# Performance work log

Measured on AMD Instinct MI355X. Metric: run time of the kernel, lower is better.

Reference implementation:

```python
import jax, jax.numpy as jnp
import numpy as np

MODES = (16, 16)
EMBED_DIM = 64
NUM_HEADS = 8


def spectral_conv(x, w):
    """FNO-style spectral conv. x: [B,S,Ci,H,W]; w: [Ci,Co,mx,my,2] (real/imag)."""
    wc = w[..., 0] + 1j * w[..., 1]
    H, W = x.shape[-2], x.shape[-1]
    mx, my = wc.shape[2], wc.shape[3]
    xf = jnp.fft.rfft2(x)                                   # [B,S,Ci,H,W//2+1]
    of = jnp.einsum('bsixy,ioxy->bsoxy', xf[..., :mx, :my], wc)
    out_f = jnp.zeros(x.shape[:2] + (wc.shape[1], H, W // 2 + 1), dtype=of.dtype)
    out_f = out_f.at[..., :mx, :my].set(of)
    return jnp.fft.irfft2(out_f, s=(H, W))


def log_cpb_bias(n_sub_x, n_sub_y, w1, b1, w2):
    """Swin-v2-style log-spaced continuous position bias -> [heads, S, S]."""
    cx = jnp.arange(n_sub_x, dtype=jnp.float32)
    cy = jnp.arange(n_sub_y, dtype=jnp.float32)
    coords = jnp.stack(jnp.meshgrid(cx, cy, indexing='ij'), axis=-1).reshape(-1, 2)
    rel = coords[:, None, :] - coords[None, :, :]           # [S,S,2]
    rel = jnp.sign(rel) * jnp.log1p(jnp.abs(rel))
    h = jax.nn.relu(rel @ w1 + b1)                          # [S,S,hidden]
    bias = h @ w2                                           # [S,S,heads]
    return jnp.transpose(bias, (2, 0, 1))


def _unflatten(f, num_heads, embed_dim):
    # [B,S,h*d,H,W] -> [B,h,S,d,H,W]
    B, S = f.shape[0], f.shape[1]
    f = f.reshape(B, S, num_heads, embed_dim, f.shape[-2], f.shape[-1])
    return jnp.transpose(f, (0, 2, 1, 3, 4, 5))


def setup_inputs() -> dict:
    key = jax.random.key(0)
    ks = jax.random.split(key, 9)
    B, S, D, H, W = 2, 64, EMBED_DIM, 32, 32
    hd = NUM_HEADS * D
    mx, my = MODES
    scale = 0.02
    return {
        'seq': jax.random.normal(ks[0], (B, S, D, H, W), dtype=jnp.float32),
        'wq': scale * jax.random.normal(ks[1], (D, hd, mx, my, 2), dtype=jnp.float32),
        'wk': scale * jax.random.normal(ks[2], (D, hd, mx, my, 2), dtype=jnp.float32),
        'wv': scale * jax.random.normal(ks[3], (D, hd, mx, my, 2), dtype=jnp.float32),
        'wo': scale * jax.random.normal(ks[4], (hd, D, mx, my, 2), dtype=jnp.float32),
        'cpb_w1': scale * jax.random.normal(ks[5], (2, D), dtype=jnp.float32),
        'cpb_b1': jnp.zeros((D,), dtype=jnp.float32),
        'cpb_w2': scale * jax.random.normal(ks[6], (D, NUM_HEADS), dtype=jnp.float32),
        'n_sub_x': 8,
        'n_sub_y': 8,
    }


def reference(seq, wq, wk, wv, wo, cpb_w1, cpb_b1, cpb_w2, n_sub_x, n_sub_y):
    q = _unflatten(spectral_conv(seq, wq), NUM_HEADS, EMBED_DIM)  # [B,h,S,d,H,W]
    k = _unflatten(spectral_conv(seq, wk), NUM_HEADS, EMBED_DIM)
    v = _unflatten(spectral_conv(seq, wv), NUM_HEADS, EMBED_DIM)

    bias = log_cpb_bias(n_sub_x, n_sub_y, cpb_w1, cpb_b1, cpb_w2)  # [h,S,S]

    d, H, W = q.shape[-3], q.shape[-2], q.shape[-1]
    scale = 1.0 / jnp.sqrt(jnp.asarray(d * H * W, dtype=q.dtype))
    scores = jnp.einsum('bhqdxy,bhkdxy->bhqk', q, k) * scale + bias[None]
    attn = jax.nn.softmax(scores, axis=-1)
    sa = jnp.einsum('bhqk,bhkdxy->bhqdxy', attn, v)          # [B,h,S,d,H,W]

    # _flatten: [B,h,S,d,H,W] -> [B,S,h*d,H,W]
    sa = jnp.transpose(sa, (0, 2, 1, 3, 4, 5))
    B, S = sa.shape[0], sa.shape[1]
    sa = sa.reshape(B, S, NUM_HEADS * EMBED_DIM, H, W)
    return spectral_conv(sa, wo)
```

## Files before the change

### kernel.cpp

```cpp
#include <hip/hip_runtime.h>

#define TWO_PI 6.28318530717958647692f

#define NH 8
#define CH 128
#define NCH 2

#define OFF_XM   0ull
#define OFF_WTA  (OFF_XM + 8388608ull)
#define OFF_WTB  (OFF_WTA + 16777216ull)
#define OFF_PO   (OFF_WTB + 16777216ull)
#define OFF_ATTN (OFF_PO + 16777216ull)
#define WS_TOTAL (OFF_ATTN + 262144ull)

typedef short bf16x8 __attribute__((ext_vector_type(8)));
typedef float f32x4 __attribute__((ext_vector_type(4)));
#define MFMA_B16(a, b, c) __builtin_amdgcn_mfma_f32_16x16x32_bf16(a, b, c, 0, 0, 0)

__device__ __forceinline__ float bl(unsigned u) { return __uint_as_float(u << 16); }
__device__ __forceinline__ unsigned short f2b(float f) {
    unsigned u = __float_as_uint(f);
    return (unsigned short)((u + 0x7fffu + ((u >> 16) & 1u)) >> 16);
}
__device__ __forceinline__ unsigned pack2(float lo, float hi) {
    return (unsigned)f2b(lo) | ((unsigned)f2b(hi) << 16);
}

__device__ __forceinline__ bf16x8 mkfrag(const unsigned* __restrict__ Wt, int co_l, int ri,
                                         int ci0, bool dc) {
    unsigned a0 = Wt[(ci0 + 0) * 64 + (co_l ^ (ci0 + 0))];
    unsigned a1 = Wt[(ci0 + 1) * 64 + (co_l ^ (ci0 + 1))];
    unsigned a2 = Wt[(ci0 + 2) * 64 + (co_l ^ (ci0 + 2))];
    unsigned a3 = Wt[(ci0 + 3) * 64 + (co_l ^ (ci0 + 3))];
    uint4 r;
    if (ri) {
        if (dc) { r.x = 0u; r.y = 0u; r.z = 0u; r.w = 0u; }
        else {
            r.x = (a0 >> 16) | (a0 << 16); r.y = (a1 >> 16) | (a1 << 16);
            r.z = (a2 >> 16) | (a2 << 16); r.w = (a3 >> 16) | (a3 << 16);
        }
    } else {
        r.x = a0 ^ 0x80000000u; r.y = a1 ^ 0x80000000u;
        r.z = a2 ^ 0x80000000u; r.w = a3 ^ 0x80000000u;
    }
    return __builtin_bit_cast(bf16x8, r);
}

__global__ __launch_bounds__(256) void k_transpose2(const float* __restrict__ srcA, unsigned* __restrict__ dstA, int kindA,
                                                    const float* __restrict__ srcB, unsigned* __restrict__ dstB, int kindB,
                                                    int m0) {
    const float* in = (blockIdx.z == 0) ? srcA : srcB;
    unsigned* outp = (blockIdx.z == 0) ? dstA : dstB;
    int kind = (blockIdx.z == 0) ? kindA : kindB;
    __shared__ unsigned T[16][65];
    int tid = threadIdx.x;
    int r0 = blockIdx.x * 64;
    int ci, h;
    if (kind == 2) { h = r0 >> 12; ci = (r0 >> 6) & 63; }
    else           { ci = r0 >> 9; h = (r0 >> 6) & 7; }
    int ml0 = blockIdx.y * 16;
    int u = (m0 + ml0) >> 4;
    const float2* in2 = (const float2*)in;
    #pragma unroll
    for (int p = 0; p < 4; ++p) {
        int f = tid + p * 256;
        int row = f >> 4, mc = f & 15;
        float fac = (kind == 0) ? (mc > 0 ? 1.41421356f : (u > 0 ? 0.70710678f : 1.f))
                  : (kind == 1) ? (mc > 0 ? 1.f : (u > 0 ? 0.5f : 1.f)) : 1.f;
        float2 v = in2[(size_t)(r0 + row) * 256 + m0 + ml0 + mc];
        T[mc][row] = pack2(v.x * fac, v.y * fac);
    }
    __syncthreads();
    #pragma unroll
    for (int p = 0; p < 4; ++p) {
        int f = tid + p * 256;
        int ml = f >> 6, co = f & 63;
        outp[((size_t)((ml0 + ml) * 8 + h) << 12) + ci * 64 + co] = T[ml][co];
    }
}

__global__ __launch_bounds__(256) void k_rfft_y(const float* __restrict__ seq,
                                                float2* __restrict__ T) {
    __shared__ float c32[32], s32[32];
    __shared__ float fld[32][33];
    int tid = threadIdx.x;
    int bc = blockIdx.x;
    if (tid < 32) { float s, c; __sincosf(TWO_PI * tid / 32.0f, &s, &c); c32[tid] = c; s32[tid] = s; }
    float4 v = ((const float4*)(seq + (size_t)bc * 1024))[tid];
    int x = tid >> 3, y4 = (tid & 7) * 4;
    fld[x][y4] = v.x; fld[x][y4 + 1] = v.y; fld[x][y4 + 2] = v.z; fld[x][y4 + 3] = v.w;
    __syncthreads();
    float2* op = T + (size_t)bc * 512;
    #pragma unroll
    for (int p = 0; p < 2; ++p) {
        int e = tid + p * 256;
        int xx = e >> 4, vv = e & 15;
        float sr = 0.f, si = 0.f;
        #pragma unroll
        for (int y = 0; y < 32; ++y) {
            float f = fld[xx][y];
            int ph = (vv * y) & 31;
            sr = fmaf(f, c32[ph], sr);
            si = fmaf(-f, s32[ph], si);
        }
        float2 t; t.x = sr; t.y = si;
        op[e] = t;
    }
}

__global__ __launch_bounds__(256) void k_rfft_x(const float2* __restrict__ T,
                                                unsigned short* __restrict__ XM) {
    __shared__ float c32[32], s32[32];
    __shared__ float2 t[8][512];
    int tid = threadIdx.x;
    int cig = blockIdx.x;
    int bs = blockIdx.y;
    if (tid < 32) { float s, c; __sincosf(TWO_PI * tid / 32.0f, &s, &c); c32[tid] = c; s32[tid] = s; }
    const float4* src = (const float4*)(T + ((size_t)bs * 64 + cig * 8) * 512);
    #pragma unroll
    for (int p = 0; p < 8; ++p) {
        int idx = tid + p * 256;
        float4 w = src[idx];
        int ch = idx >> 8, r2 = idx & 255;
        float2 t0; t0.x = w.x; t0.y = w.y;
        float2 t1; t1.x = w.z; t1.y = w.w;
        t[ch][r2 * 2] = t0; t[ch][r2 * 2 + 1] = t1;
    }
    __syncthreads();
    int u = tid >> 4, vv = tid & 15;
    unsigned outw[8];
    for (int ch = 0; ch < 8; ++ch) {
        float xr = 0.f, xi = 0.f;
        #pragma unroll
        for (int x = 0; x < 32; ++x) {
            float2 tv = t[ch][x * 16 + vv];
            int ph = (u * x) & 31;
            float c = c32[ph], s = s32[ph];
            xr += tv.x * c + tv.y * s;
            xi += tv.y * c - tv.x * s;
        }
        outw[ch] = pack2(xr, xi);
    }
    uint4* op = (uint4*)(XM + (((size_t)tid * 128 + bs) * 64 + cig * 8) * 2);
    uint4 a, b;
    a.x = outw[0]; a.y = outw[1]; a.z = outw[2]; a.w = outw[3];
    b.x = outw[4]; b.y = outw[5]; b.z = outw[6]; b.w = outw[7];
    op[0] = a; op[1] = b;
}

__global__ __launch_bounds__(512) void k_qks(const unsigned short* __restrict__ XM,
                                             const unsigned* __restrict__ WQ,
                                             const unsigned* __restrict__ WK,
                                             float* __restrict__ part, int mbase) {
    __shared__ __align__(16) unsigned char Xs[16384];
    __shared__ __align__(16) unsigned Wq[4096];
    __shared__ __align__(16) unsigned Wk[4096];
    __shared__ __align__(16) unsigned char Qs[16384];
    __shared__ __align__(16) unsigned char Ks[16384];
    int tid = threadIdx.x;
    int mg = blockIdx.x, h = blockIdx.y, b = blockIdx.z;
    int lane = tid & 63, w = tid >> 6;
    int lr = lane & 15, lg = lane >> 4;
    int wr = w & 1, wc = w >> 1;
    int sxa = (lr & 7) << 4;
    int ri = lr & 1;
    f32x4 zf = {0.f, 0.f, 0.f, 0.f};
    f32x4 sacc[2];
    sacc[0] = zf; sacc[1] = zf;
    for (int mm = 0; mm < 4; ++mm) {
        int ml = mg * 4 + mm;
        int mode = mbase + ml;
        bool dc = (mode == 0);
        __syncthreads();
        {
            const unsigned short* xg = XM + ((size_t)mode * 128 + b * 64) * 128;
            #pragma unroll
            for (int p = 0; p < 2; ++p) {
                int g = tid + p * 512; int row = g >> 4, c16 = g & 15;
                uint4 v = *(const uint4*)(xg + row * 128 + c16 * 8);
                *(uint4*)(Xs + row * 256 + ((c16 * 16) ^ ((row & 7) << 4))) = v;
            }
        }
        {
            const unsigned* tq = WQ + ((size_t)(ml * 8 + h) << 12);
            const unsigned* tk = WK + ((size_t)(ml * 8 + h) << 12);
            #pragma unroll
            for (int p = 0; p < 16; ++p) {
                int idx = tid + p * 512;
                int r = idx & 4095;
                int ci = r >> 6, co = r & 63;
                if (idx < 4096) Wq[ci * 64 + (co ^ ci)] = tq[r];
                else            Wk[ci * 64 + (co ^ ci)] = tk[r];
            }
        }
        __syncthreads();
        {
            f32x4 qa[2][2], ka[2][2];
            #pragma unroll
            for (int m = 0; m < 2; ++m)
                #pragma unroll
                for (int n = 0; n < 2; ++n) { qa[m][n] = zf; ka[m][n] = zf; }
            #pragma unroll
            for (int ks = 0; ks < 4; ++ks) {
                int kb = (ks * 64 + lg * 16) ^ sxa;
                int ci0 = ks * 16 + lg * 4;
                bf16x8 a0 = *(const bf16x8*)(Xs + (wr * 32 + lr) * 256 + kb);
                bf16x8 a1 = *(const bf16x8*)(Xs + (wr * 32 + 16 + lr) * 256 + kb);
                #pragma unroll
                for (int n = 0; n < 2; ++n) {
                    int co_l = wc * 16 + n * 8 + (lr >> 1);
                    bf16x8 bq = mkfrag(Wq, co_l, ri, ci0, dc);
                    bf16x8 bk = mkfrag(Wk, co_l, ri, ci0, dc);
                    qa[0][n] = MFMA_B16(a0, bq, qa[0][n]);
                    qa[1][n] = MFMA_B16(a1, bq, qa[1][n]);
                    ka[0][n] = MFMA_B16(a0, bk, ka[0][n]);
                    ka[1][n] = MFMA_B16(a1, bk, ka[1][n]);
                }
            }
            #pragma unroll
            for (int m = 0; m < 2; ++m)
                #pragma unroll
                for (int n = 0; n < 2; ++n) {
                    int colb = (wc * 32 + n * 16 + lr) * 2;
                    #pragma unroll
                    for (int r = 0; r < 4; ++r) {
                        int row = wr * 32 + m * 16 + lg * 4 + r;
                        int swz = (row & 7) << 4;
                        *(unsigned short*)(Qs + row * 256 + (colb ^ swz)) = f2b(qa[m][n][r]);
                        *(unsigned short*)(Ks + row * 256 + (colb ^ swz)) = f2b(ka[m][n][r]);
                    }
                }
        }
        __syncthreads();
        {
            #pragma unroll
            for (int ks = 0; ks < 4; ++ks) {
                int kb = (ks * 64 + lg * 16) ^ sxa;
                bf16x8 a0 = *(const bf16x8*)(Qs + (wr * 32 + lr) * 256 + kb);
                bf16x8 a1 = *(const bf16x8*)(Qs + (wr * 32 + 16 + lr) * 256 + kb);
                bf16x8 b0 = *(const bf16x8*)(Ks + (wc * 16 + lr) * 256 + kb);
                sacc[0] = MFMA_B16(a0, b0, sacc[0]);
                sacc[1] = MFMA_B16(a1, b0, sacc[1]);
            }
        }
    }
    float* pp = part + (((size_t)((mbase >> 2) + mg) * 16 + b * 8 + h) << 12);
    #pragma unroll
    for (int m = 0; m < 2; ++m)
        #pragma unroll
        for (int r = 0; r < 4; ++r)
            pp[(wr * 32 + m * 16 + lg * 4 + r) * 64 + wc * 16 + lr] = sacc[m][r];
}

__global__ void k_softmax(const float* __restrict__ part,
                          const float* __restrict__ w1, const float* __restrict__ b1,
                          const float* __restrict__ w2, unsigned short* __restrict__ attnb) {
    int j = threadIdx.x;
    int i = blockIdx.x;
    int bh = blockIdx.y;
    int h = bh & 7;
    float s = 0.f;
    for (int mg = 0; mg < 64; ++mg)
        s += part[(((size_t)mg * 16 + bh) * 64 + i) * 64 + j];
    float dx = (float)((i >> 3) - (j >> 3));
    float dy = (float)((i & 7) - (j & 7));
    float rx = (dx > 0.f ? 1.f : (dx < 0.f ? -1.f : 0.f)) * log1pf(fabsf(dx));
    float ry = (dy > 0.f ? 1.f : (dy < 0.f ? -1.f : 0.f)) * log1pf(fabsf(dy));
    float bias = 0.f;
    for (int l = 0; l < 64; ++l) {
        float hv = fmaxf(rx * w1[l] + ry * w1[64 + l] + b1[l], 0.f);
        bias = fmaf(hv, w2[l * NH + h], bias);
    }
    s = s * (1.0f / 262144.0f) + bias;
    float m = s;
    for (int o = 32; o >= 1; o >>= 1) m = fmaxf(m, __shfl_xor(m, o));
    float e = expf(s - m);
    float t = e;
    for (int o = 32; o >= 1; o >>= 1) t += __shfl_xor(t, o);
    attnb[((size_t)bh * 64 + i) * 64 + j] = f2b(e / t);
}

__global__ __launch_bounds__(512) void k_savo(const unsigned short* __restrict__ XM,
                                              const unsigned* __restrict__ WV,
                                              const unsigned* __restrict__ WO,
                                              const unsigned short* __restrict__ attnb,
                                              float* __restrict__ outf, int mbase) {
    __shared__ __align__(16) unsigned char Xs[16384];
    __shared__ __align__(16) unsigned Wv[4096];
    __shared__ __align__(16) unsigned Wo[4096];
    __shared__ __align__(16) unsigned char Vt[16384];
    __shared__ __align__(16) unsigned char Ss[16384];
    int tid = threadIdx.x;
    int ml = blockIdx.x, b = blockIdx.y;
    int mode = mbase + ml;
    bool dc = (mode == 0);
    int lane = tid & 63, w = tid >> 6;
    int lr = lane & 15, lg = lane >> 4;
    int wr = w & 1, wc = w >> 1;
    int sxa = (lr & 7) << 4;
    int ri = lr & 1;
    f32x4 zf = {0.f, 0.f, 0.f, 0.f};
    {
        const unsigned short* xg = XM + ((size_t)mode * 128 + b * 64) * 128;
        #pragma unroll
        for (int p = 0; p < 2; ++p) {
            int g = tid + p * 512; int row = g >> 4, c16 = g & 15;
            uint4 v = *(const uint4*)(xg + row * 128 + c16 * 8);
            *(uint4*)(Xs + row * 256 + ((c16 * 16) ^ ((row & 7) << 4))) = v;
        }
    }
    f32x4 oacc[2][2];
    oacc[0][0] = zf; oacc[0][1] = zf; oacc[1][0] = zf; oacc[1][1] = zf;
    for (int h = 0; h < NH; ++h) {
        __syncthreads();
        {
            const unsigned* tv = WV + ((size_t)(ml * 8 + h) << 12);
            const unsigned* to = WO + ((size_t)(ml * 8 + h) << 12);
            #pragma unroll
            for (int p = 0; p < 16; ++p) {
                int idx = tid + p * 512;
                int r = idx & 4095;
                int ci = r >> 6, co = r & 63;
                if (idx < 4096) Wv[ci * 64 + (co ^ ci)] = tv[r];
                else            Wo[ci * 64 + (co ^ ci)] = to[r];
            }
        }
        bf16x8 af[2][2];
        #pragma unroll
        for (int m = 0; m < 2; ++m)
            #pragma unroll
            for (int ks = 0; ks < 2; ++ks) {
                int irow = wr * 32 + m * 16 + lr;
                af[m][ks] = *(const bf16x8*)(attnb + (((size_t)(b * 8 + h) * 64 + irow) * 64 + ks * 32 + lg * 8));
            }
        __syncthreads();
        {
            f32x4 va[2][2];
            va[0][0] = zf; va[0][1] = zf; va[1][0] = zf; va[1][1] = zf;
            #pragma unroll
            for (int ks = 0; ks < 4; ++ks) {
                int kb = (ks * 64 + lg * 16) ^ sxa;
                int ci0 = ks * 16 + lg * 4;
                bf16x8 a0 = *(const bf16x8*)(Xs + (wr * 32 + lr) * 256 + kb);
                bf16x8 a1 = *(const bf16x8*)(Xs + (wr * 32 + 16 + lr) * 256 + kb);
                #pragma unroll
                for (int n = 0; n < 2; ++n) {
                    int co_l = wc * 16 + n * 8 + (lr >> 1);
                    bf16x8 bb = mkfrag(Wv, co_l, ri, ci0, dc);
                    va[0][n] = MFMA_B16(a0, bb, va[0][n]);
                    va[1][n] = MFMA_B16(a1, bb, va[1][n]);
                }
            }
            #pragma unroll
            for (int m = 0; m < 2; ++m)
                #pragma unroll
                for (int n = 0; n < 2; ++n) {
                    int cp = wc * 32 + n * 16 + lr;
                    int j0 = wr * 32 + m * 16 + lg * 4;
                    uint2 t;
                    t.x = pack2(va[m][n][0], va[m][n][1]);
                    t.y = pack2(va[m][n][2], va[m][n][3]);
                    *(uint2*)(Vt + cp * 128 + ((j0 * 2) ^ ((cp & 7) << 4))) = t;
                }
        }
        __syncthreads();
        {
            f32x4 sa_[2][2];
            sa_[0][0] = zf; sa_[0][1] = zf; sa_[1][0] = zf; sa_[1][1] = zf;
            #pragma unroll
            for (int ks = 0; ks < 2; ++ks) {
                #pragma unroll
                for (int n = 0; n < 2; ++n) {
                    int cp = wc * 32 + n * 16 + lr;
                    bf16x8 bb = *(const bf16x8*)(Vt + cp * 128 + ((ks * 64 + lg * 16) ^ ((cp & 7) << 4)));
                    sa_[0][n] = MFMA_B16(af[0][ks], bb, sa_[0][n]);
                    sa_[1][n] = MFMA_B16(af[1][ks], bb, sa_[1][n]);
                }
            }
            #pragma unroll
            for (int m = 0; m < 2; ++m)
                #pragma unroll
                for (int n = 0; n < 2; ++n) {
                    int colb = (wc * 32 + n * 16 + lr) * 2;
                    #pragma unroll
                    for (int r = 0; r < 4; ++r) {
                        int row = wr * 32 + m * 16 + lg * 4 + r;
                        *(unsigned short*)(Ss + row * 256 + (colb ^ ((row & 7) << 4))) = f2b(sa_[m][n][r]);
                    }
                }
        }
        __syncthreads();
        {
            #pragma unroll
            for (int ks = 0; ks < 4; ++ks) {
                int kb = (ks * 64 + lg * 16) ^ sxa;
                int ci0 = ks * 16 + lg * 4;
                bf16x8 a0 = *(const bf16x8*)(Ss + (wr * 32 + lr) * 256 + kb);
                bf16x8 a1 = *(const bf16x8*)(Ss + (wr * 32 + 16 + lr) * 256 + kb);
                #pragma unroll
                for (int n = 0; n < 2; ++n) {
                    int co_l = wc * 16 + n * 8 + (lr >> 1);
                    bf16x8 bb = mkfrag(Wo, co_l, ri, ci0, false);
                    oacc[0][n] = MFMA_B16(a0, bb, oacc[0][n]);
                    oacc[1][n] = MFMA_B16(a1, bb, oacc[1][n]);
                }
            }
        }
    }
    #pragma unroll
    for (int m = 0; m < 2; ++m)
        #pragma unroll
        for (int n = 0; n < 2; ++n)
            #pragma unroll
            for (int r = 0; r < 4; ++r) {
                int i = wr * 32 + m * 16 + lg * 4 + r;
                int c2p = wc * 32 + n * 16 + lr;
                outf[((size_t)mode * 128 + b * 64 + i) * 128 + c2p] = oacc[m][n][r];
            }
}

__global__ __launch_bounds__(256) void k_irfft(const float* __restrict__ outf,
                                               float* __restrict__ out) {
    __shared__ float c32[32], s32[32];
    __shared__ float mf[256][18];
    __shared__ float sr[16 * 33], si[16 * 33];
    int tid = threadIdx.x;
    int cg = blockIdx.x;
    int bs = blockIdx.y;
    if (tid < 32) { float s, c; __sincosf(TWO_PI * tid / 32.0f, &s, &c); c32[tid] = c; s32[tid] = s; }
    {
        const float4* gp = (const float4*)(outf + (((size_t)tid * 128 + bs) * 64 + cg * 8) * 2);
        for (int q = 0; q < 4; ++q) {
            float4 v = gp[q];
            mf[tid][q * 4 + 0] = v.x; mf[tid][q * 4 + 1] = v.y;
            mf[tid][q * 4 + 2] = v.z; mf[tid][q * 4 + 3] = v.w;
        }
    }
    __syncthreads();
    for (int cc = 0; cc < 8; ++cc) {
        for (int p = 0; p < 2; ++p) {
            int e = tid + p * 256;
            int u = e >> 5, y = e & 31;
            float fr0 = mf[u * 16][cc * 2];
            float fi0 = (u == 0) ? 0.f : mf[u * 16][cc * 2 + 1];
            float ssr = 0.5f * fr0, ssi = 0.5f * fi0;
            for (int v = 1; v < 16; ++v) {
                float fr = mf[u * 16 + v][cc * 2], fi = mf[u * 16 + v][cc * 2 + 1];
                int ph = (v * y) & 31;
                float c = c32[ph], s = s32[ph];
                ssr += fr * c - fi * s;
                ssi += fr * s + fi * c;
            }
            sr[u * 33 + y] = ssr; si[u * 33 + y] = ssi;
        }
        __syncthreads();
        float res[4];
        for (int p = 0; p < 4; ++p) {
            int pos = tid + p * 256;
            int x = pos >> 5, y = pos & 31;
            float acc = 0.f;
            for (int u = 0; u < 16; ++u) {
                int ph = (u * x) & 31;
                acc += sr[u * 33 + y] * c32[ph] - si[u * 33 + y] * s32[ph];
            }
            res[p] = acc * (1.0f / 512.0f);
        }
        float* op = out + ((size_t)(bs * 64 + cg * 8 + cc)) * 1024;
        for (int p = 0; p < 4; ++p) op[tid + p * 256] = res[p];
        __syncthreads();
    }
}

extern "C" void kernel_launch(void* const* d_in, const int* in_sizes, int n_in,
                              void* d_out, int out_size, void* d_ws, size_t ws_size,
                              hipStream_t stream) {
    (void)in_sizes; (void)n_in; (void)out_size;
    const float* seq = (const float*)d_in[0];
    const float* wq = (const float*)d_in[1];
    const float* wk = (const float*)d_in[2];
    const float* wv = (const float*)d_in[3];
    const float* wo = (const float*)d_in[4];
    const float* cw1 = (const float*)d_in[5];
    const float* cb1 = (const float*)d_in[6];
    const float* cw2 = (const float*)d_in[7];
    float* out = (float*)d_out;
    char* ws = (char*)d_ws;
    if (ws_size < WS_TOTAL) return;

    unsigned short* XM = (unsigned short*)(ws + OFF_XM);
    unsigned* WTA = (unsigned*)(ws + OFF_WTA);
    unsigned* WTB = (unsigned*)(ws + OFF_WTB);
    float2* Tbuf = (float2*)(ws + OFF_WTA);
    float* PART = (float*)(ws + OFF_PO);
    float* OUTF = (float*)(ws + OFF_PO);
    unsigned short* ATTNB = (unsigned short*)(ws + OFF_ATTN);

    k_rfft_y<<<dim3(8192), dim3(256), 0, stream>>>(seq, Tbuf);
    k_rfft_x<<<dim3(8, 128), dim3(256), 0, stream>>>(Tbuf, XM);

    for (int c = 0; c < NCH; ++c) {
        int m0 = c * CH;
        k_transpose2<<<dim3(512, CH / 16, 2), dim3(256), 0, stream>>>(wq, WTA, 0, wk, WTB, 0, m0);
        k_qks<<<dim3(CH / 4, NH, 2), dim3(512), 0, stream>>>(XM, WTA, WTB, PART, m0);
    }
    k_softmax<<<dim3(64, 16), dim3(64), 0, stream>>>(PART, cw1, cb1, cw2, ATTNB);

    for (int c = 0; c < NCH; ++c) {
        int m0 = c * CH;
        k_transpose2<<<dim3(512, CH / 16, 2), dim3(256), 0, stream>>>(wv, WTA, 1, wo, WTB, 2, m0);
        k_savo<<<dim3(CH, 2), dim3(512), 0, stream>>>(XM, WTA, WTB, ATTNB, OUTF, m0);
    }
    k_irfft<<<dim3(8, 128), dim3(256), 0, stream>>>(OUTF, out);
}
```

Baseline: 353.9 us.

## Split inverse FFT into two kernels to remove per-channel block barriers

Splits the fused inverse real FFT into two kernels. The first does the y-direction partial sums for all 8 channels at once and writes them to a global scratch buffer. The second reloads them and does the x-direction sum with fully unrolled loops. This removes the per-channel __syncthreads loop and serial structure of the old kernel. In exchange it adds a global round trip, an extra launch, and more shared-memory use.

```diff
diff --git a/kernel.cpp b/kernel.cpp
--- a/kernel.cpp
+++ b/kernel.cpp
@@ -419,55 +419,80 @@
             }
 }
 
-__global__ __launch_bounds__(256) void k_irfft(const float* __restrict__ outf,
-                                               float* __restrict__ out) {
+__global__ __launch_bounds__(256) void k_irfft_v(const float* __restrict__ outf,
+                                                 float2* __restrict__ G) {
     __shared__ float c32[32], s32[32];
-    __shared__ float mf[256][18];
-    __shared__ float sr[16 * 33], si[16 * 33];
+    __shared__ float2 mf[256][8];
     int tid = threadIdx.x;
     int cg = blockIdx.x;
     int bs = blockIdx.y;
     if (tid < 32) { float s, c; __sincosf(TWO_PI * tid / 32.0f, &s, &c); c32[tid] = c; s32[tid] = s; }
-    {
-        const float4* gp = (const float4*)(outf + (((size_t)tid * 128 + bs) * 64 + cg * 8) * 2);
-        for (int q = 0; q < 4; ++q) {
-            float4 v = gp[q];
-            mf[tid][q * 4 + 0] = v.x; mf[tid][q * 4 + 1] = v.y;
-            mf[tid][q * 4 + 2] = v.z; mf[tid][q * 4 + 3] = v.w;
-        }
+    #pragma unroll
+    for (int p = 0; p < 4; ++p) {
+        int idx = tid + p * 256;
+        int mode = idx >> 2, q = idx & 3;
+        float4 v = *(const float4*)(outf + ((size_t)mode * 128 + bs) * 128 + cg * 16 + q * 4);
+        float2 t0; t0.x = v.x; t0.y = v.y;
+        float2 t1; t1.x = v.z; t1.y = v.w;
+        mf[mode][q * 2] = t0; mf[mode][q * 2 + 1] = t1;
     }
     __syncthreads();
-    for (int cc = 0; cc < 8; ++cc) {
-        for (int p = 0; p < 2; ++p) {
-            int e = tid + p * 256;
-            int u = e >> 5, y = e & 31;
-            float fr0 = mf[u * 16][cc * 2];
-            float fi0 = (u == 0) ? 0.f : mf[u * 16][cc * 2 + 1];
+    #pragma unroll
+    for (int p = 0; p < 2; ++p) {
+        int e = tid + p * 256;
+        int u = e >> 5, y = e & 31;
+        #pragma unroll
+        for (int ch = 0; ch < 8; ++ch) {
+            float2 f0 = mf[u * 16][ch];
+            float fr0 = f0.x;
+            float fi0 = (u == 0) ? 0.f : f0.y;
             float ssr = 0.5f * fr0, ssi = 0.5f * fi0;
             for (int v = 1; v < 16; ++v) {
-                float fr = mf[u * 16 + v][cc * 2], fi = mf[u * 16 + v][cc * 2 + 1];
+                float2 f = mf[u * 16 + v][ch];
                 int ph = (v * y) & 31;
                 float c = c32[ph], s = s32[ph];
-                ssr += fr * c - fi * s;
-                ssi += fr * s + fi * c;
-            }
-            sr[u * 33 + y] = ssr; si[u * 33 + y] = ssi;
-        }
-        __syncthreads();
-        float res[4];
-        for (int p = 0; p < 4; ++p) {
-            int pos = tid + p * 256;
-            int x = pos >> 5, y = pos & 31;
+                ssr += f.x * c - f.y * s;
+                ssi += f.x * s + f.y * c;
+            }
+            float2 g; g.x = ssr; g.y = ssi;
+            G[(((size_t)u * 128 + bs) * 64 + cg * 8 + ch) * 32 + y] = g;
+        }
+    }
+}
+
+__global__ __launch_bounds__(256) void k_irfft_u(const float2* __restrict__ G,
+                                                 float* __restrict__ out) {
+    __shared__ float c32[32], s32[32];
+    __shared__ float2 Gs[16][8][32];
+    int tid = threadIdx.x;
+    int cg = blockIdx.x;
+    int bs = blockIdx.y;
+    if (tid < 32) { float s, c; __sincosf(TWO_PI * tid / 32.0f, &s, &c); c32[tid] = c; s32[tid] = s; }
+    #pragma unroll
+    for (int p = 0; p < 8; ++p) {
+        int idx = tid + p * 256;
+        int y2 = idx & 15, ch = (idx >> 4) & 7, u = idx >> 7;
+        float4 v = *(const float4*)((const float*)G + ((((size_t)u * 128 + bs) * 64 + cg * 8 + ch) * 32 + y2 * 2) * 2);
+        float2 t0; t0.x = v.x; t0.y = v.y;
+        float2 t1; t1.x = v.z; t1.y = v.w;
+        Gs[u][ch][y2 * 2] = t0; Gs[u][ch][y2 * 2 + 1] = t1;
+    }
+    __syncthreads();
+    #pragma unroll
+    for (int p = 0; p < 4; ++p) {
+        int pos = tid + p * 256;
+        int x = pos >> 5, y = pos & 31;
+        #pragma unroll
+        for (int ch = 0; ch < 8; ++ch) {
             float acc = 0.f;
+            #pragma unroll
             for (int u = 0; u < 16; ++u) {
+                float2 g = Gs[u][ch][y];
                 int ph = (u * x) & 31;
-                acc += sr[u * 33 + y] * c32[ph] - si[u * 33 + y] * s32[ph];
-            }
-            res[p] = acc * (1.0f / 512.0f);
-        }
-        float* op = out + ((size_t)(bs * 64 + cg * 8 + cc)) * 1024;
-        for (int p = 0; p < 4; ++p) op[tid + p * 256] = res[p];
-        __syncthreads();
+                acc += g.x * c32[ph] - g.y * s32[ph];
+            }
+            out[((size_t)(bs * 64 + cg * 8 + ch)) * 1024 + x * 32 + y] = acc * (1.0f / 512.0f);
+        }
     }
 }
 
@@ -491,6 +516,7 @@
     unsigned* WTA = (unsigned*)(ws + OFF_WTA);
     unsigned* WTB = (unsigned*)(ws + OFF_WTB);
     float2* Tbuf = (float2*)(ws + OFF_WTA);
+    float2* G = (float2*)(ws + OFF_WTA);
     float* PART = (float*)(ws + OFF_PO);
     float* OUTF = (float*)(ws + OFF_PO);
     unsigned short* ATTNB = (unsigned short*)(ws + OFF_ATTN);
@@ -510,5 +536,6 @@
         k_transpose2<<<dim3(512, CH / 16, 2), dim3(256), 0, stream>>>(wv, WTA, 1, wo, WTB, 2, m0);
         k_savo<<<dim3(CH, 2), dim3(512), 0, stream>>>(XM, WTA, WTB, ATTNB, OUTF, m0);
     }
-    k_irfft<<<dim3(8, 128), dim3(256), 0, stream>>>(OUTF, out);
-}
+    k_irfft_v<<<dim3(8, 128), dim3(256), 0, stream>>>(OUTF, G);
+    k_irfft_u<<<dim3(8, 128), dim3(256), 0, stream>>>(G, out);
+}
```

After: 522.8 us. 1.48x slower.
